# Kernel tuning notes

Measured on AMD Instinct MI355X. Metric: run time of the kernel, lower is better.

The kernel has to match this reference:

```python
import jax, jax.numpy as jnp
import numpy as np


def _shift(w):
    # max(0, -min(w)): scalar shift making w + shift non-negative
    return jnp.maximum(0.0, -jnp.min(w))


def shifted_linear(x, W, b=None):
    # F.linear with non-negative weights plus row-sum correction
    alpha = _shift(W)
    y = x @ (W + alpha).T - alpha * jnp.sum(x, axis=-1, keepdims=True)
    if b is not None:
        y = y + b
    return y


def shifted_depthwise_conv(x, w, b):
    # x: (B, D, L), w: (D, 1, K) depthwise; causal-style padding K-1, sliced to L by caller
    alpha = _shift(w)
    k = w.shape[2]
    pad = k - 1
    dn = ('NCH', 'OIH', 'NCH')
    groups = w.shape[0]
    y = jax.lax.conv_general_dilated(x, w + alpha, (1,), [(pad, pad)],
                                     dimension_numbers=dn, feature_group_count=groups)
    ones_k = jnp.ones_like(w)
    ssum = jax.lax.conv_general_dilated(x, ones_k, (1,), [(pad, pad)],
                                        dimension_numbers=dn, feature_group_count=groups)
    return y - alpha * ssum + b[None, :, None]


def setup_inputs() -> dict:
    key = jax.random.key(0)
    ks = jax.random.split(key, 10)
    d_model, d_inner, d_state, d_conv, dt_rank = 1024, 2048, 16, 4, 64
    B, L = 2, 1024
    s = 0.05
    return {
        'hidden_states': jax.random.normal(ks[0], (B, L, d_model), jnp.float32),
        'W_in': jax.random.normal(ks[1], (2 * d_inner, d_model), jnp.float32) * s,
        'conv_w': jax.random.normal(ks[2], (d_inner, 1, d_conv), jnp.float32) * 0.3,
        'conv_b': jax.random.normal(ks[3], (d_inner,), jnp.float32) * s,
        'W_x': jax.random.normal(ks[4], (dt_rank + 2 * d_state, d_inner), jnp.float32) * s,
        'W_dt': jax.random.normal(ks[5], (d_inner, dt_rank), jnp.float32) * s,
        'dt_bias': jax.random.normal(ks[6], (d_inner,), jnp.float32),
        'W_out': jax.random.normal(ks[7], (d_model, d_inner), jnp.float32) * s,
        'A_log': jax.random.normal(ks[8], (d_inner, d_state), jnp.float32) * 0.5,
        'D': jax.random.normal(ks[9], (d_inner,), jnp.float32),
    }


def reference(hidden_states, W_in, conv_w, conv_b, W_x, W_dt, dt_bias, W_out, A_log, D):
    b, l, dm = hidden_states.shape
    d_inner = conv_w.shape[0]
    d_state = A_log.shape[1]
    dt_rank = W_dt.shape[1]

    A = jnp.exp(A_log)  # (d_inner, d_state), always positive

    # in_proj over (b*l, d_model) -> (b, 2*d_inner, l)
    xz = shifted_linear(hidden_states.reshape(b * l, dm), W_in)
    xz = xz.reshape(b, l, 2 * d_inner).transpose(0, 2, 1)
    x, z = xz[:, :d_inner], xz[:, d_inner:]

    # depthwise shifted conv + SiLU activation, truncated to seqlen
    x = jax.nn.silu(shifted_depthwise_conv(x, conv_w, conv_b)[..., :l])

    # x_proj -> dt_raw, B, C
    x_dbl = shifted_linear(x.transpose(0, 2, 1).reshape(b * l, d_inner), W_x)
    dt_raw = x_dbl[:, :dt_rank]
    Bm = x_dbl[:, dt_rank:dt_rank + d_state].reshape(b, l, d_state).transpose(0, 2, 1)  # (b,n,l)
    Cm = x_dbl[:, dt_rank + d_state:].reshape(b, l, d_state).transpose(0, 2, 1)         # (b,n,l)
    dt = shifted_linear(dt_raw, W_dt).reshape(b, l, d_inner).transpose(0, 2, 1)          # (b,d,l)

    # delta activation (softplus) with bias, clamped
    delta = jnp.clip(jax.nn.softplus(dt + dt_bias[None, :, None]), 1e-4, 20.0)

    # global scalar shifts for B and C
    beta = _shift(Bm)
    gamma = _shift(Cm)
    B_nn = Bm + beta
    C_nn = Cm + gamma

    # precomputed per-step operands, scan axis first: (l, b, d, n)
    deltaA = jnp.exp(-jnp.einsum('bdl,dn->lbdn', delta, A))
    dBu = jnp.einsum('bdl,bnl,bdl->lbdn', delta, B_nn, x)
    C_scan = C_nn.transpose(2, 0, 1)  # (l, b, n)

    def step(xc, inp):
        dA_i, dBu_i, C_i = inp
        xc = dA_i * xc + dBu_i                                   # (b,d,n)
        y = jnp.einsum('bdn,bn->bd', xc, C_i) - gamma * jnp.sum(xc, axis=-1)
        return xc, y

    x0 = jnp.zeros((b, d_inner, d_state), dtype=delta.dtype)
    _, ys = jax.lax.scan(step, x0, (deltaA, dBu, C_scan))        # ys: (l, b, d)

    y = ys.transpose(1, 2, 0) + x * D[None, :, None]             # (b, d, l) skip term
    y = y * jax.nn.silu(z)                                       # gate activation

    out = shifted_linear(y.transpose(0, 2, 1).reshape(b * l, d_inner), W_out)
    return out.reshape(b, l, dm)
```

## Files before the change

### kernel.cpp

```cpp
#include <hip/hip_runtime.h>
#include <hip/hip_bf16.h>
#include <math.h>

#define DM 1024
#define DI 2048
#define DS 16
#define DTR 64
#define NB 2
#define LL 1024
#define TT (NB*LL)
#define SCH 16
#define NCH (LL/SCH)

typedef unsigned short u16;
typedef __attribute__((ext_vector_type(8))) short bf16x8;
typedef __attribute__((ext_vector_type(4))) float f32x4;

#define LOG2E 1.4426950408889634f

__device__ inline u16 f2bf(float f) {
  union { float f; unsigned u; } c; c.f = f;
  unsigned u = c.u;
  return (u16)((u + 0x7fffu + ((u >> 16) & 1u)) >> 16);
}
__device__ inline float bf2f(u16 u) {
  union { unsigned u; float f; } c; c.u = ((unsigned)u) << 16;
  return c.f;
}

#define GLDS16(g, l) __builtin_amdgcn_global_load_lds( \
    (const __attribute__((address_space(1))) unsigned int*)(g), \
    (__attribute__((address_space(3))) unsigned int*)(l), 16, 0, 0)

template<int BM, int BN, int EPI, int OB>
__global__ __launch_bounds__(256) void gemm_bf16(
    const u16* __restrict__ A, const u16* __restrict__ B,
    void* __restrict__ Cv, int M, int N, int K, int kpb,
    const float* __restrict__ bias) {
  constexpr int WAVES_M = BM / 64;
  constexpr int WAVES_N = 4 / WAVES_M;
  constexpr int WTM = 4;
  constexpr int WTN = BN / (WAVES_N * 16);
  constexpr int ASLABS = BM / 16;
  constexpr int SLABS = (BM + BN) / 16;
  constexpr int SPW = SLABS / 4;
  __shared__ u16 As[BM * 32];
  __shared__ u16 Bs[BN * 32];
  const int tid = threadIdx.x;
  const int wave = tid >> 6;
  const int lane = tid & 63;
  const int bm = blockIdx.y * BM;
  const int bn = blockIdx.x * BN;
  const int wm = (wave / WAVES_N) * 64;
  const int wn = (wave % WAVES_N) * (WTN * 16);
  const int r4 = lane >> 2;
  const int kc = (lane & 3) * 8;
  const int fr = lane & 15;
  const int fq = lane >> 4;
  const int koff = blockIdx.z * kpb;
  float* C = (float*)Cv + (size_t)blockIdx.z * M * N;
  u16* C16 = (u16*)Cv;

  f32x4 acc[WTM][WTN];
#pragma unroll
  for (int i = 0; i < WTM; ++i)
#pragma unroll
    for (int j = 0; j < WTN; ++j) acc[i][j] = (f32x4){0.f, 0.f, 0.f, 0.f};

  for (int k0 = koff; k0 < koff + kpb; k0 += 32) {
#pragma unroll
    for (int s = wave * SPW; s < (wave + 1) * SPW; ++s) {
      if (s < ASLABS) {
        int row = s * 16 + r4;
        GLDS16(A + (size_t)(bm + row) * K + k0 + kc, &As[s * 512]);
      } else {
        int row = (s - ASLABS) * 16 + r4;
        GLDS16(B + (size_t)(bn + row) * K + k0 + kc, &Bs[(s - ASLABS) * 512]);
      }
    }
    __syncthreads();
    bf16x8 af[WTM], bf[WTN];
#pragma unroll
    for (int i = 0; i < WTM; ++i)
      af[i] = *(const bf16x8*)&As[(wm + 16 * i + fr) * 32 + fq * 8];
#pragma unroll
    for (int j = 0; j < WTN; ++j)
      bf[j] = *(const bf16x8*)&Bs[(wn + 16 * j + fr) * 32 + fq * 8];
#pragma unroll
    for (int i = 0; i < WTM; ++i)
#pragma unroll
      for (int j = 0; j < WTN; ++j)
        acc[i][j] = __builtin_amdgcn_mfma_f32_16x16x32_bf16(af[i], bf[j], acc[i][j], 0, 0, 0);
    __syncthreads();
  }

#pragma unroll
  for (int i = 0; i < WTM; ++i) {
    int row0 = bm + wm + 16 * i + fq * 4;
#pragma unroll
    for (int j = 0; j < WTN; ++j) {
      int col = bn + wn + 16 * j + fr;
#pragma unroll
      for (int r = 0; r < 4; ++r) {
        float v = acc[i][j][r];
        if (EPI == 1) {
          v += bias[col];
          float sp = (v > 20.0f) ? v : log1pf(expf(v));
          v = fminf(fmaxf(sp, 1e-4f), 20.0f);
        }
        if (OB == 1) C16[(size_t)(row0 + r) * N + col] = f2bf(v);
        else         C[(size_t)(row0 + r) * N + col] = v;
      }
    }
  }
}

__global__ __launch_bounds__(256) void gemm3_reduce(
    const float* __restrict__ part, float* __restrict__ xdb,
    u16* __restrict__ dtraw_bf, float* __restrict__ pmin) {
  int i = blockIdx.x * 256 + threadIdx.x;
  int t = i >> 7, col = i & 127;
  float s = 0.f;
#pragma unroll
  for (int z = 0; z < 16; ++z) s += part[(size_t)z * TT * 128 + i];
  if (col < 96) xdb[t * 96 + col] = s;
  if (col < 64) dtraw_bf[t * 64 + col] = f2bf(s);
  float mn = (col >= 64 && col < 80) ? s : 3.4e38f;
#pragma unroll
  for (int o = 32; o; o >>= 1) mn = fminf(mn, __shfl_down(mn, o));
  __shared__ float sm[4];
  if ((threadIdx.x & 63) == 0) sm[threadIdx.x >> 6] = mn;
  __syncthreads();
  if (threadIdx.x == 0)
    pmin[blockIdx.x] = fminf(fminf(sm[0], sm[1]), fminf(sm[2], sm[3]));
}

__global__ __launch_bounds__(256) void beta_fin(
    const float* __restrict__ pmin, float* __restrict__ beta) {
  float mn = 3.4e38f;
#pragma unroll
  for (int k = 0; k < 4; ++k) mn = fminf(mn, pmin[threadIdx.x + 256 * k]);
#pragma unroll
  for (int o = 32; o; o >>= 1) mn = fminf(mn, __shfl_down(mn, o));
  __shared__ float sm[4];
  if ((threadIdx.x & 63) == 0) sm[threadIdx.x >> 6] = mn;
  __syncthreads();
  if (threadIdx.x == 0)
    beta[0] = fmaxf(0.0f, -fminf(fminf(sm[0], sm[1]), fminf(sm[2], sm[3])));
}

__global__ __launch_bounds__(256) void cast_all(
    const float* __restrict__ hs, const float* __restrict__ win,
    const float* __restrict__ wout, const float* __restrict__ wx,
    const float* __restrict__ wdt,
    u16* __restrict__ hs_bf, u16* __restrict__ win_bf,
    u16* __restrict__ wout_bf, u16* __restrict__ wx_bf,
    u16* __restrict__ wdt_bf) {
  int gid = blockIdx.x * 256 + threadIdx.x;
  const float* src; u16* dst; int off;
  if (gid < 524288)       { src = hs;   dst = hs_bf;   off = gid; }
  else if (gid < 1572864) { src = win;  dst = win_bf;  off = gid - 524288; }
  else if (gid < 2097152) { src = wout; dst = wout_bf; off = gid - 1572864; }
  else if (gid < 2146304) { src = wx;   dst = wx_bf;   off = gid - 2097152; }
  else if (gid < 2179072) { src = wdt;  dst = wdt_bf;  off = gid - 2146304; }
  else {
    ushort4 z4 = {0, 0, 0, 0};
    ((ushort4*)wx_bf)[49152 + gid - 2179072] = z4;
    return;
  }
  float4 v = ((const float4*)src)[off];
  ushort4 o;
  o.x = f2bf(v.x); o.y = f2bf(v.y); o.z = f2bf(v.z); o.w = f2bf(v.w);
  ((ushort4*)dst)[off] = o;
}

__global__ __launch_bounds__(256) void conv_silu4(
    const u16* __restrict__ xz, const float* __restrict__ w,
    const float* __restrict__ cb, u16* __restrict__ xc_bf) {
  int gid = blockIdx.x * 256 + threadIdx.x;
  int dq = (gid & 511) * 4;
  int t = gid >> 9;
  int l = t & (LL - 1);
  float wv[4][4];
#pragma unroll
  for (int j = 0; j < 4; ++j) {
    float4 ww = *(const float4*)&w[(dq + j) * 4];
    wv[j][0] = ww.x; wv[j][1] = ww.y; wv[j][2] = ww.z; wv[j][3] = ww.w;
  }
  float4 acc = *(const float4*)&cb[dq];
#pragma unroll
  for (int k = 0; k < 4; ++k) {
    int ll = l - 3 + k;
    if (ll < 0) continue;
    ushort4 xv = *(const ushort4*)&xz[(size_t)(t - 3 + k) * (2 * DI) + dq];
    acc.x += bf2f(xv.x) * wv[0][k]; acc.y += bf2f(xv.y) * wv[1][k];
    acc.z += bf2f(xv.z) * wv[2][k]; acc.w += bf2f(xv.w) * wv[3][k];
  }
  acc.x /= (1.0f + expf(-acc.x)); acc.y /= (1.0f + expf(-acc.y));
  acc.z /= (1.0f + expf(-acc.z)); acc.w /= (1.0f + expf(-acc.w));
  ushort4 o;
  o.x = f2bf(acc.x); o.y = f2bf(acc.y); o.z = f2bf(acc.z); o.w = f2bf(acc.w);
  *(ushort4*)&xc_bf[(size_t)t * DI + dq] = o;
}

__global__ __launch_bounds__(256) void scan_pass1(
    const float* __restrict__ delta, const u16* __restrict__ xc_bf,
    const float* __restrict__ xdb, const float* __restrict__ A_log,
    const float* __restrict__ beta_p,
    float* __restrict__ hend, float* __restrict__ Ssum) {
  const int d = blockIdx.x * 256 + threadIdx.x;
  const int c = blockIdx.y;
  const int b = blockIdx.z;
  __shared__ float Bsh[SCH][16];
  const float beta = beta_p[0];
  const int t0 = b * LL + c * SCH;
  {
    int i = threadIdx.x;
    int tt = i >> 4, n = i & 15;
    Bsh[tt][n] = xdb[(size_t)(t0 + tt) * 96 + 64 + n] + beta;
  }
  __syncthreads();
  float Av2[16];
#pragma unroll
  for (int n = 0; n < 16; ++n) Av2[n] = expf(A_log[d * 16 + n]) * LOG2E;
  float h[16];
#pragma unroll
  for (int n = 0; n < 16; ++n) h[n] = 0.f;
  float S = 0.f;
  for (int tt = 0; tt < SCH; ++tt) {
    int t = t0 + tt;
    float dv = delta[(size_t)t * DI + d];
    float xv = bf2f(xc_bf[(size_t)t * DI + d]);
    float dx = dv * xv;
    S += dv;
#pragma unroll
    for (int n = 0; n < 16; ++n) {
      float a = __builtin_amdgcn_exp2f(-dv * Av2[n]);
      h[n] = a * h[n] + dx * Bsh[tt][n];
    }
  }
  size_t base = (((size_t)(b * NCH + c) * DI) + d) * 16;
#pragma unroll
  for (int n = 0; n < 16; ++n) hend[base + n] = h[n];
  Ssum[((size_t)(b * NCH + c) * DI) + d] = S;
}

__global__ __launch_bounds__(256) void scan_pass2(
    float* __restrict__ hend, const float* __restrict__ Ssum,
    const float* __restrict__ A_log) {
  int gid = blockIdx.x * 256 + threadIdx.x;
  int n = gid & 15;
  int d = (gid >> 4) & (DI - 1);
  int b = gid >> 15;
  float Av2 = expf(A_log[d * 16 + n]) * LOG2E;
  float H = 0.f;
  for (int c = 0; c < NCH; ++c) {
    size_t cb = ((size_t)(b * NCH + c) * DI) + d;
    float hl = hend[cb * 16 + n];
    float p = __builtin_amdgcn_exp2f(-Av2 * Ssum[cb]);
    hend[cb * 16 + n] = H;
    H = p * H + hl;
  }
}

__global__ __launch_bounds__(256) void scan_pass3(
    const float* __restrict__ delta, const u16* __restrict__ xc_bf,
    const float* __restrict__ xdb, const u16* __restrict__ xz_bf,
    const float* __restrict__ A_log, const float* __restrict__ Dp,
    const float* __restrict__ beta_p, const float* __restrict__ hstart,
    u16* __restrict__ ybf) {
  const int d = blockIdx.x * 256 + threadIdx.x;
  const int c = blockIdx.y;
  const int b = blockIdx.z;
  __shared__ float Bsh[SCH][16];
  __shared__ float Csh[SCH][16];
  const float beta = beta_p[0];
  const int t0 = b * LL + c * SCH;
  {
    int i = threadIdx.x;
    int tt = i >> 4, n = i & 15;
    size_t row = (size_t)(t0 + tt) * 96;
    Bsh[tt][n] = xdb[row + 64 + n] + beta;
    Csh[tt][n] = xdb[row + 80 + n];
  }
  __syncthreads();
  float Av2[16];
#pragma unroll
  for (int n = 0; n < 16; ++n) Av2[n] = expf(A_log[d * 16 + n]) * LOG2E;
  float h[16];
  size_t base = (((size_t)(b * NCH + c) * DI) + d) * 16;
#pragma unroll
  for (int n = 0; n < 16; ++n) h[n] = hstart[base + n];
  const float Dd = Dp[d];
  for (int tt = 0; tt < SCH; ++tt) {
    int t = t0 + tt;
    float dv = delta[(size_t)t * DI + d];
    float xv = bf2f(xc_bf[(size_t)t * DI + d]);
    float dx = dv * xv;
    float yv = 0.f;
#pragma unroll
    for (int n = 0; n < 16; ++n) {
      float a = __builtin_amdgcn_exp2f(-dv * Av2[n]);
      h[n] = a * h[n] + dx * Bsh[tt][n];
      yv += h[n] * Csh[tt][n];
    }
    float zv = bf2f(xz_bf[(size_t)t * (2 * DI) + DI + d]);
    float out = (yv + xv * Dd) * (zv / (1.0f + expf(-zv)));
    ybf[(size_t)t * DI + d] = f2bf(out);
  }
}

extern "C" void kernel_launch(void* const* d_in, const int* in_sizes, int n_in,
                              void* d_out, int out_size, void* d_ws, size_t ws_size,
                              hipStream_t stream) {
  const float* hs      = (const float*)d_in[0];
  const float* W_in    = (const float*)d_in[1];
  const float* conv_w  = (const float*)d_in[2];
  const float* conv_b  = (const float*)d_in[3];
  const float* W_x     = (const float*)d_in[4];
  const float* W_dt    = (const float*)d_in[5];
  const float* dt_bias = (const float*)d_in[6];
  const float* W_out   = (const float*)d_in[7];
  const float* A_log   = (const float*)d_in[8];
  const float* Dp      = (const float*)d_in[9];
  float* out = (float*)d_out;

  float* ws       = (float*)d_ws;
  float* xz_bfR   = ws;
  float* xcv_bfR  = xz_bfR + (size_t)TT * 2 * DI / 2;
  float* xdb      = xcv_bfR + (size_t)TT * DI / 2;
  float* dlt      = xdb + (size_t)TT * 96;
  float* betab    = dlt + (size_t)TT * DI;
  float* pmin     = betab + 64;
  float* hend     = pmin + 1024;
  float* Ssum     = hend + (size_t)NB * NCH * DI * 16;
  float* hs_bfR   = Ssum + (size_t)NB * NCH * DI;
  float* win_bfR  = hs_bfR + (size_t)TT * DM / 2;
  float* wout_bfR = win_bfR + (size_t)2 * DI * DM / 2;
  float* wx_bfR   = wout_bfR + (size_t)DM * DI / 2;
  float* wdt_bfR  = wx_bfR + 131072;
  float* dtraw_bfR = wdt_bfR + 65536;

  u16* xz_bf    = (u16*)xz_bfR;
  u16* xcv_bf   = (u16*)xcv_bfR;
  u16* hs_bf    = (u16*)hs_bfR;
  u16* win_bf   = (u16*)win_bfR;
  u16* wout_bf  = (u16*)wout_bfR;
  u16* wx_bf    = (u16*)wx_bfR;
  u16* wdt_bf   = (u16*)wdt_bfR;
  u16* dtraw_bf = (u16*)dtraw_bfR;
  u16* ybf      = (u16*)win_bfR;
  float* part   = dlt;

  dim3 blk(256);

  cast_all<<<8576, blk, 0, stream>>>(hs, W_in, W_out, W_x, W_dt,
                                     hs_bf, win_bf, wout_bf, wx_bf, wdt_bf);

  gemm_bf16<128, 128, 0, 1><<<dim3(4096 / 128, TT / 128), blk, 0, stream>>>(
      hs_bf, win_bf, xz_bf, TT, 2 * DI, DM, DM, nullptr);

  conv_silu4<<<(TT * DI / 4) / 256, blk, 0, stream>>>(xz_bf, conv_w, conv_b, xcv_bf);

  gemm_bf16<128, 128, 0, 0><<<dim3(1, TT / 128, 16), blk, 0, stream>>>(
      xcv_bf, wx_bf, part, TT, 128, DI, 128, nullptr);
  gemm3_reduce<<<1024, blk, 0, stream>>>(part, xdb, dtraw_bf, pmin);

  beta_fin<<<1, blk, 0, stream>>>(pmin, betab);

  gemm_bf16<128, 128, 1, 0><<<dim3(DI / 128, TT / 128), blk, 0, stream>>>(
      dtraw_bf, wdt_bf, dlt, TT, DI, DTR, DTR, dt_bias);

  scan_pass1<<<dim3(DI / 256, NCH, NB), blk, 0, stream>>>(
      dlt, xcv_bf, xdb, A_log, betab, hend, Ssum);
  scan_pass2<<<(NB * DI * DS) / 256, blk, 0, stream>>>(hend, Ssum, A_log);
  scan_pass3<<<dim3(DI / 256, NCH, NB), blk, 0, stream>>>(
      dlt, xcv_bf, xdb, xz_bf, A_log, Dp, betab, hend, ybf);

  gemm_bf16<64, 128, 0, 0><<<dim3(DM / 128, TT / 64), blk, 0, stream>>>(
      ybf, wout_bf, out, TT, DM, DI, DI, nullptr);
}
```

Measured before the change: 267.9 us.

## Store delta in bf16, fuse beta reduction via atomicMin, retune tiles and scan chunk

Delta is now written by the dt GEMM as bf16 instead of fp32 and read back as bf16 in both scan passes, halving that traffic. The separate beta_fin kernel is removed; each reduce block instead does an atomicMin on an order-preserving float key, which cast_all initialises. The split-K for the x-projection drops from 16 to 8 planes with smaller M tiles. GEMM tile shapes change for the in, dt and out projections, and the scan chunk length doubles, halving the number of chunks carried in pass 2. Lower delta precision may affect accuracy.

```diff
diff --git a/kernel.cpp b/kernel.cpp
--- a/kernel.cpp
+++ b/kernel.cpp
@@ -9,8 +9,9 @@
 #define NB 2
 #define LL 1024
 #define TT (NB*LL)
-#define SCH 16
+#define SCH 32
 #define NCH (LL/SCH)
+#define KPLANES 8
 
 typedef unsigned short u16;
 typedef __attribute__((ext_vector_type(8))) short bf16x8;
@@ -25,6 +26,16 @@
 }
 __device__ inline float bf2f(u16 u) {
   union { unsigned u; float f; } c; c.u = ((unsigned)u) << 16;
+  return c.f;
+}
+
+__device__ inline unsigned fkey(float f) {
+  union { float f; unsigned u; } c; c.f = f;
+  return (c.u & 0x80000000u) ? ~c.u : (c.u | 0x80000000u);
+}
+__device__ inline float funkey(unsigned k) {
+  union { unsigned u; float f; } c;
+  c.u = (k & 0x80000000u) ? (k & 0x7fffffffu) : ~k;
   return c.f;
 }
 
@@ -117,12 +128,12 @@
 
 __global__ __launch_bounds__(256) void gemm3_reduce(
     const float* __restrict__ part, float* __restrict__ xdb,
-    u16* __restrict__ dtraw_bf, float* __restrict__ pmin) {
+    u16* __restrict__ dtraw_bf, unsigned* __restrict__ betakey) {
   int i = blockIdx.x * 256 + threadIdx.x;
   int t = i >> 7, col = i & 127;
   float s = 0.f;
 #pragma unroll
-  for (int z = 0; z < 16; ++z) s += part[(size_t)z * TT * 128 + i];
+  for (int z = 0; z < KPLANES; ++z) s += part[(size_t)z * TT * 128 + i];
   if (col < 96) xdb[t * 96 + col] = s;
   if (col < 64) dtraw_bf[t * 64 + col] = f2bf(s);
   float mn = (col >= 64 && col < 80) ? s : 3.4e38f;
@@ -131,22 +142,10 @@
   __shared__ float sm[4];
   if ((threadIdx.x & 63) == 0) sm[threadIdx.x >> 6] = mn;
   __syncthreads();
-  if (threadIdx.x == 0)
-    pmin[blockIdx.x] = fminf(fminf(sm[0], sm[1]), fminf(sm[2], sm[3]));
-}
-
-__global__ __launch_bounds__(256) void beta_fin(
-    const float* __restrict__ pmin, float* __restrict__ beta) {
-  float mn = 3.4e38f;
-#pragma unroll
-  for (int k = 0; k < 4; ++k) mn = fminf(mn, pmin[threadIdx.x + 256 * k]);
-#pragma unroll
-  for (int o = 32; o; o >>= 1) mn = fminf(mn, __shfl_down(mn, o));
-  __shared__ float sm[4];
-  if ((threadIdx.x & 63) == 0) sm[threadIdx.x >> 6] = mn;
-  __syncthreads();
-  if (threadIdx.x == 0)
-    beta[0] = fmaxf(0.0f, -fminf(fminf(sm[0], sm[1]), fminf(sm[2], sm[3])));
+  if (threadIdx.x == 0) {
+    float m = fminf(fminf(sm[0], sm[1]), fminf(sm[2], sm[3]));
+    atomicMin(betakey, fkey(m));
+  }
 }
 
 __global__ __launch_bounds__(256) void cast_all(
@@ -155,8 +154,9 @@
     const float* __restrict__ wdt,
     u16* __restrict__ hs_bf, u16* __restrict__ win_bf,
     u16* __restrict__ wout_bf, u16* __restrict__ wx_bf,
-    u16* __restrict__ wdt_bf) {
+    u16* __restrict__ wdt_bf, unsigned* __restrict__ betakey) {
   int gid = blockIdx.x * 256 + threadIdx.x;
+  if (gid == 0) betakey[0] = 0xFFFFFFFFu;
   const float* src; u16* dst; int off;
   if (gid < 524288)       { src = hs;   dst = hs_bf;   off = gid; }
   else if (gid < 1572864) { src = win;  dst = win_bf;  off = gid - 524288; }
@@ -204,18 +204,17 @@
 }
 
 __global__ __launch_bounds__(256) void scan_pass1(
-    const float* __restrict__ delta, const u16* __restrict__ xc_bf,
+    const u16* __restrict__ delta, const u16* __restrict__ xc_bf,
     const float* __restrict__ xdb, const float* __restrict__ A_log,
-    const float* __restrict__ beta_p,
+    const unsigned* __restrict__ betak,
     float* __restrict__ hend, float* __restrict__ Ssum) {
   const int d = blockIdx.x * 256 + threadIdx.x;
   const int c = blockIdx.y;
   const int b = blockIdx.z;
   __shared__ float Bsh[SCH][16];
-  const float beta = beta_p[0];
+  const float beta = fmaxf(0.0f, -funkey(betak[0]));
   const int t0 = b * LL + c * SCH;
-  {
-    int i = threadIdx.x;
+  for (int i = threadIdx.x; i < SCH * 16; i += 256) {
     int tt = i >> 4, n = i & 15;
     Bsh[tt][n] = xdb[(size_t)(t0 + tt) * 96 + 64 + n] + beta;
   }
@@ -229,7 +228,7 @@
   float S = 0.f;
   for (int tt = 0; tt < SCH; ++tt) {
     int t = t0 + tt;
-    float dv = delta[(size_t)t * DI + d];
+    float dv = bf2f(delta[(size_t)t * DI + d]);
     float xv = bf2f(xc_bf[(size_t)t * DI + d]);
     float dx = dv * xv;
     S += dv;
@@ -264,20 +263,19 @@
 }
 
 __global__ __launch_bounds__(256) void scan_pass3(
-    const float* __restrict__ delta, const u16* __restrict__ xc_bf,
+    const u16* __restrict__ delta, const u16* __restrict__ xc_bf,
     const float* __restrict__ xdb, const u16* __restrict__ xz_bf,
     const float* __restrict__ A_log, const float* __restrict__ Dp,
-    const float* __restrict__ beta_p, const float* __restrict__ hstart,
+    const unsigned* __restrict__ betak, const float* __restrict__ hstart,
     u16* __restrict__ ybf) {
   const int d = blockIdx.x * 256 + threadIdx.x;
   const int c = blockIdx.y;
   const int b = blockIdx.z;
   __shared__ float Bsh[SCH][16];
   __shared__ float Csh[SCH][16];
-  const float beta = beta_p[0];
+  const float beta = fmaxf(0.0f, -funkey(betak[0]));
   const int t0 = b * LL + c * SCH;
-  {
-    int i = threadIdx.x;
+  for (int i = threadIdx.x; i < SCH * 16; i += 256) {
     int tt = i >> 4, n = i & 15;
     size_t row = (size_t)(t0 + tt) * 96;
     Bsh[tt][n] = xdb[row + 64 + n] + beta;
@@ -294,7 +292,7 @@
   const float Dd = Dp[d];
   for (int tt = 0; tt < SCH; ++tt) {
     int t = t0 + tt;
-    float dv = delta[(size_t)t * DI + d];
+    float dv = bf2f(delta[(size_t)t * DI + d]);
     float xv = bf2f(xc_bf[(size_t)t * DI + d]);
     float dx = dv * xv;
     float yv = 0.f;
@@ -329,10 +327,10 @@
   float* xz_bfR   = ws;
   float* xcv_bfR  = xz_bfR + (size_t)TT * 2 * DI / 2;
   float* xdb      = xcv_bfR + (size_t)TT * DI / 2;
-  float* dlt      = xdb + (size_t)TT * 96;
-  float* betab    = dlt + (size_t)TT * DI;
-  float* pmin     = betab + 64;
-  float* hend     = pmin + 1024;
+  float* dlt_bfR  = xdb + (size_t)TT * 96;
+  float* part     = dlt_bfR + (size_t)TT * DI / 2;
+  float* betab    = part + (size_t)KPLANES * TT * 128;
+  float* hend     = betab + 64;
   float* Ssum     = hend + (size_t)NB * NCH * DI * 16;
   float* hs_bfR   = Ssum + (size_t)NB * NCH * DI;
   float* win_bfR  = hs_bfR + (size_t)TT * DM / 2;
@@ -343,40 +341,40 @@
 
   u16* xz_bf    = (u16*)xz_bfR;
   u16* xcv_bf   = (u16*)xcv_bfR;
+  u16* dlt_bf   = (u16*)dlt_bfR;
   u16* hs_bf    = (u16*)hs_bfR;
   u16* win_bf   = (u16*)win_bfR;
   u16* wout_bf  = (u16*)wout_bfR;
   u16* wx_bf    = (u16*)wx_bfR;
   u16* wdt_bf   = (u16*)wdt_bfR;
   u16* dtraw_bf = (u16*)dtraw_bfR;
+  unsigned* betakey = (unsigned*)betab;
   u16* ybf      = (u16*)win_bfR;
-  float* part   = dlt;
 
   dim3 blk(256);
 
   cast_all<<<8576, blk, 0, stream>>>(hs, W_in, W_out, W_x, W_dt,
-                                     hs_bf, win_bf, wout_bf, wx_bf, wdt_bf);
-
-  gemm_bf16<128, 128, 0, 1><<<dim3(4096 / 128, TT / 128), blk, 0, stream>>>(
+                                     hs_bf, win_bf, wout_bf, wx_bf, wdt_bf,
+                                     betakey);
+
+  gemm_bf16<128, 64, 0, 1><<<dim3(4096 / 64, TT / 128), blk, 0, stream>>>(
       hs_bf, win_bf, xz_bf, TT, 2 * DI, DM, DM, nullptr);
 
   conv_silu4<<<(TT * DI / 4) / 256, blk, 0, stream>>>(xz_bf, conv_w, conv_b, xcv_bf);
 
-  gemm_bf16<128, 128, 0, 0><<<dim3(1, TT / 128, 16), blk, 0, stream>>>(
-      xcv_bf, wx_bf, part, TT, 128, DI, 128, nullptr);
-  gemm3_reduce<<<1024, blk, 0, stream>>>(part, xdb, dtraw_bf, pmin);
-
-  beta_fin<<<1, blk, 0, stream>>>(pmin, betab);
-
-  gemm_bf16<128, 128, 1, 0><<<dim3(DI / 128, TT / 128), blk, 0, stream>>>(
-      dtraw_bf, wdt_bf, dlt, TT, DI, DTR, DTR, dt_bias);
+  gemm_bf16<64, 128, 0, 0><<<dim3(1, TT / 64, KPLANES), blk, 0, stream>>>(
+      xcv_bf, wx_bf, part, TT, 128, DI, DI / KPLANES, nullptr);
+  gemm3_reduce<<<1024, blk, 0, stream>>>(part, xdb, dtraw_bf, betakey);
+
+  gemm_bf16<64, 128, 1, 1><<<dim3(DI / 128, TT / 64), blk, 0, stream>>>(
+      dtraw_bf, wdt_bf, dlt_bf, TT, DI, DTR, DTR, dt_bias);
 
   scan_pass1<<<dim3(DI / 256, NCH, NB), blk, 0, stream>>>(
-      dlt, xcv_bf, xdb, A_log, betab, hend, Ssum);
+      dlt_bf, xcv_bf, xdb, A_log, betakey, hend, Ssum);
   scan_pass2<<<(NB * DI * DS) / 256, blk, 0, stream>>>(hend, Ssum, A_log);
   scan_pass3<<<dim3(DI / 256, NCH, NB), blk, 0, stream>>>(
-      dlt, xcv_bf, xdb, xz_bf, A_log, Dp, betab, hend, ybf);
-
-  gemm_bf16<64, 128, 0, 0><<<dim3(DM / 128, TT / 64), blk, 0, stream>>>(
+      dlt_bf, xcv_bf, xdb, xz_bf, A_log, Dp, betakey, hend, ybf);
+
+  gemm_bf16<64, 64, 0, 0><<<dim3(DM / 64, TT / 64), blk, 0, stream>>>(
       ybf, wout_bf, out, TT, DM, DI, DI, nullptr);
 }
```

Measured after the change: 270.5 us. About the same (+1.0%).
